# Kernel tuning notes

Hardware: AMD Instinct MI355X
Metric: run time of the kernel (lower is better)

The kernel has to match this reference:

```python
import jax, jax.numpy as jnp
import numpy as np

HEAD = 16

def setup_inputs() -> dict:
    key = jax.random.key(0)
    kq, kk, kv = jax.random.split(key, 3)
    B, S, D = 2, 2048, 1024
    q = jax.random.normal(kq, (B, S, D), dtype=jnp.float32)
    k = jax.random.normal(kk, (B, S, D), dtype=jnp.float32)
    v = jax.random.normal(kv, (B, S, D), dtype=jnp.float32)
    return {"q": q, "k": k, "v": v}

def reference(q, k, v):
    # NOTE: the source module overwrites the projected q1/k1/v1 with the raw
    # inputs (q1 = q, etc.), so w_q/w_k/w_v/w_o never affect the output.
    B, S, D = q.shape
    H = HEAD
    hd = D // H
    # [B, S, D] -> [B, H, S, hd]
    qh = q.reshape(B, S, H, hd).transpose(0, 2, 1, 3)
    kh = k.reshape(B, S, H, hd).transpose(0, 2, 1, 3)
    vh = v.reshape(B, S, H, hd).transpose(0, 2, 1, 3)
    scale = 1.0 / jnp.sqrt(jnp.float32(hd))
    scores = jnp.einsum('bhqd,bhkd->bhqk', qh, kh) * scale  # [B, H, S, S]
    attn = jax.nn.softmax(scores, axis=-1)
    x = jnp.einsum('bhqk,bhkd->bhqd', attn, vh)             # [B, H, S, hd]
    return x.transpose(0, 2, 1, 3).reshape(B, S, D)
```

## Files before the change

### kernel.cpp

```cpp
#include <hip/hip_runtime.h>
#include <hip/hip_bf16.h>

typedef __attribute__((ext_vector_type(8)))  __bf16 bf16x8;
typedef __attribute__((ext_vector_type(4)))  __bf16 bf16x4;
typedef __attribute__((ext_vector_type(4)))  float  f32x4;
typedef __attribute__((ext_vector_type(16))) float  f32x16;

#define S_LEN    2048
#define D_MODEL  1024
#define NH       16
#define HD       64
#define QB       128
#define NTILE    32
#define NOUTER   16
#define C_SCALE  0.18033688011112042f

static __device__ __forceinline__ f32x16 mfma32(bf16x8 a, bf16x8 b, f32x16 c) {
    return __builtin_amdgcn_mfma_f32_32x32x16_bf16(a, b, c, 0, 0, 0);
}

static __device__ __forceinline__ void gload16(const void* g, void* l) {
    __builtin_amdgcn_global_load_lds(
        (const __attribute__((address_space(1))) void*)g,
        (__attribute__((address_space(3)))       void*)l, 16, 0, 0);
}

__global__ __launch_bounds__(256, 4)
void prep_kernel(const float* __restrict__ Kp, const float* __restrict__ Vp,
                 char* __restrict__ Kb, char* __restrict__ Vb)
{
    const int bid  = blockIdx.x;
    const int bh   = bid >> 5;
    const int tile = bid & 31;
    const int b = bh >> 4, h = bh & 15;
    const int tid = threadIdx.x;
    const size_t gbase = (size_t)b * S_LEN * D_MODEL + (size_t)h * HD;
    char* kout = Kb + (size_t)bid * 8192;
    char* vout = Vb + (size_t)bid * 8192;

    {
        const int krow = tid >> 2, c2 = tid & 3;
        const float* kp = Kp + gbase + (size_t)(tile * 64 + krow) * D_MODEL + c2 * 16;
        f32x4 x0 = *(const f32x4*)(kp);
        f32x4 x1 = *(const f32x4*)(kp + 4);
        f32x4 x2 = *(const f32x4*)(kp + 8);
        f32x4 x3 = *(const f32x4*)(kp + 12);
        bf16x8 f0, f1;
        #pragma unroll
        for (int j = 0; j < 4; ++j) {
            f0[j] = (__bf16)x0[j]; f0[j + 4] = (__bf16)x1[j];
            f1[j] = (__bf16)x2[j]; f1[j + 4] = (__bf16)x3[j];
        }
        const int sw = (krow & 7) << 4;
        *(bf16x8*)(kout + krow * 128 + ((c2 * 32)      ^ sw)) = f0;
        *(bf16x8*)(kout + krow * 128 + ((c2 * 32 + 16) ^ sw)) = f1;
    }
    {
        const int vkg = tid >> 4, vdg = tid & 15;
        const float* vp = Vp + gbase + (size_t)(tile * 64 + vkg * 4) * D_MODEL + vdg * 4;
        f32x4 r0 = *(const f32x4*)(vp);
        f32x4 r1 = *(const f32x4*)(vp + D_MODEL);
        f32x4 r2 = *(const f32x4*)(vp + 2 * D_MODEL);
        f32x4 r3 = *(const f32x4*)(vp + 3 * D_MODEL);
        const int kvoff = 8 * ((vkg >> 1) & 1) + 16 * (vkg & 1) + 32 * (vkg >> 2);
        #pragma unroll
        for (int c = 0; c < 4; ++c) {
            const int d = vdg * 4 + c;
            bf16x4 pk;
            pk[0] = (__bf16)r0[c]; pk[1] = (__bf16)r1[c];
            pk[2] = (__bf16)r2[c]; pk[3] = (__bf16)r3[c];
            *(bf16x4*)(vout + d * 128 + (kvoff ^ ((d & 7) << 4))) = pk;
        }
    }
}

__global__ __launch_bounds__(1024, 4)
void attn_kernel(const float* __restrict__ Qp, const char* __restrict__ Kb,
                 const char* __restrict__ Vb, float* __restrict__ Op)
{
    __shared__ __align__(16) char smem[65536];

    const int bid = blockIdx.x;
    const int bh = bid & 31, qtile = bid >> 5;
    const int b = bh >> 4, h = bh & 15;
    const int tid = threadIdx.x;
    const int w = tid >> 6, lane = tid & 63;
    const int ql = lane & 31, hi = lane >> 5;
    const int qs = w & 3, kq = w >> 2;

    const size_t gbase = (size_t)b * S_LEN * D_MODEL + (size_t)h * HD;

    bf16x8 qf[4];
    {
        const int qrow = qtile * QB + qs * 32 + ql;
        const float* qp = Qp + gbase + (size_t)qrow * D_MODEL + hi * 8;
        #pragma unroll
        for (int ks = 0; ks < 4; ++ks) {
            f32x4 a = *(const f32x4*)(qp + ks * 16);
            f32x4 c = *(const f32x4*)(qp + ks * 16 + 4);
            bf16x8 f;
            #pragma unroll
            for (int j = 0; j < 4; ++j) {
                f[j]     = (__bf16)(a[j] * C_SCALE);
                f[j + 4] = (__bf16)(c[j] * C_SCALE);
            }
            qf[ks] = f;
        }
    }

    const char* kg0 = Kb + (size_t)(bh * NTILE) * 8192;
    const char* vg0 = Vb + (size_t)(bh * NTILE) * 8192;

    auto stage = [&](int db, int t) {
        const char* kg = kg0 + (size_t)t * 16384;
        const char* vg = vg0 + (size_t)t * 16384;
        char* kl = smem + db * 16384;
        char* vl = smem + 32768 + db * 16384;
        const int o = w * 1024;
        gload16(kg + o + lane * 16, kl + o);
        gload16(vg + o + lane * 16, vl + o);
    };

    const int tb = (kq >> 1) * 8192;
    const int rl = 32 * (kq & 1);
    const int vc = 64 * (kq & 1);

    f32x16 oa = {0,0,0,0,0,0,0,0,0,0,0,0,0,0,0,0};
    f32x16 ob = {0,0,0,0,0,0,0,0,0,0,0,0,0,0,0,0};
    f32x4 l4 = {0.f, 0.f, 0.f, 0.f};

    stage(0, 0);
    int cur = 0;
    for (int t = 0; t < NOUTER; ++t) {
        __syncthreads();
        if (t + 1 < NOUTER) stage(cur ^ 1, t + 1);

        const char* kl = smem + cur * 16384 + tb;
        const char* vl = smem + 32768 + cur * 16384 + tb;

        f32x16 s = {0,0,0,0,0,0,0,0,0,0,0,0,0,0,0,0};
        __builtin_amdgcn_s_setprio(1);
        #pragma unroll
        for (int ks = 0; ks < 4; ++ks) {
            const int row = rl + ql;
            bf16x8 k0 = *(const bf16x8*)(kl + row * 128 +
                            ((32 * ks + 16 * hi) ^ ((ql & 7) << 4)));
            s = mfma32(k0, qf[ks], s);
        }
        __builtin_amdgcn_s_setprio(0);

        bf16x8 pa[2];
        {
            float p[16];
            #pragma unroll
            for (int i = 0; i < 16; ++i) {
                p[i] = __builtin_amdgcn_exp2f(s[i]);
                l4[i & 3] += p[i];
            }
            #pragma unroll
            for (int z = 0; z < 2; ++z) {
                bf16x8 f;
                #pragma unroll
                for (int j = 0; j < 8; ++j) f[j] = (__bf16)p[z * 8 + j];
                pa[z] = f;
            }
        }

        __builtin_amdgcn_s_setprio(1);
        #pragma unroll
        for (int ks2 = 0; ks2 < 2; ++ks2) {
            const int col = vc + 32 * ks2 + 16 * hi;
            const int d0 = ql, d1 = 32 + ql;
            bf16x8 v0 = *(const bf16x8*)(vl + d0 * 128 + (col ^ ((d0 & 7) << 4)));
            bf16x8 v1 = *(const bf16x8*)(vl + d1 * 128 + (col ^ ((d1 & 7) << 4)));
            oa = mfma32(pa[ks2], v0, oa);
            ob = mfma32(pa[ks2], v1, ob);
        }
        __builtin_amdgcn_s_setprio(0);
        cur ^= 1;
    }

    float lsum = (l4[0] + l4[1]) + (l4[2] + l4[3]);
    lsum += __shfl_xor(lsum, 32);
    __syncthreads();
    float* lbuf  = (float*)smem;
    float* lbuf2 = (float*)(smem + 2048);
    float* obuf  = (float*)(smem + 4096);
    if (lane < 32) lbuf[kq * 128 + qs * 32 + ql] = lsum;
    __syncthreads();
    if (kq == 1) {
        if (lane < 32) {
            const int idx = qs * 32 + ql;
            lbuf2[idx] = lbuf[idx] + lbuf[128 + idx] + lbuf[256 + idx] + lbuf[384 + idx];
        }
        #pragma unroll
        for (int i = 0; i < 16; ++i) {
            const int qloc = (i & 3) + 8 * (i >> 2) + 4 * hi;
            obuf[qs * 2048 + qloc * 64 + ql]      = oa[i];
            obuf[qs * 2048 + qloc * 64 + 32 + ql] = ob[i];
        }
    }
    __syncthreads();
    if (kq == 0) {
        #pragma unroll
        for (int i = 0; i < 16; ++i) {
            const int qloc = (i & 3) + 8 * (i >> 2) + 4 * hi;
            oa[i] += obuf[qs * 2048 + qloc * 64 + ql];
            ob[i] += obuf[qs * 2048 + qloc * 64 + 32 + ql];
        }
    }
    __syncthreads();
    if (kq == 2) {
        #pragma unroll
        for (int i = 0; i < 16; ++i) {
            const int qloc = (i & 3) + 8 * (i >> 2) + 4 * hi;
            obuf[qs * 2048 + qloc * 64 + ql]      = oa[i];
            obuf[qs * 2048 + qloc * 64 + 32 + ql] = ob[i];
        }
    }
    __syncthreads();
    if (kq == 0) {
        #pragma unroll
        for (int i = 0; i < 16; ++i) {
            const int qloc = (i & 3) + 8 * (i >> 2) + 4 * hi;
            oa[i] += obuf[qs * 2048 + qloc * 64 + ql];
            ob[i] += obuf[qs * 2048 + qloc * 64 + 32 + ql];
        }
    }
    __syncthreads();
    if (kq == 3) {
        #pragma unroll
        for (int i = 0; i < 16; ++i) {
            const int qloc = (i & 3) + 8 * (i >> 2) + 4 * hi;
            obuf[qs * 2048 + qloc * 64 + ql]      = oa[i];
            obuf[qs * 2048 + qloc * 64 + 32 + ql] = ob[i];
        }
    }
    __syncthreads();
    if (kq == 0) {
        #pragma unroll
        for (int i = 0; i < 16; ++i) {
            const int qloc = (i & 3) + 8 * (i >> 2) + 4 * hi;
            const float inv = 1.0f / lbuf2[qs * 32 + qloc];
            const float v0 = (oa[i] + obuf[qs * 2048 + qloc * 64 + ql])      * inv;
            const float v1 = (ob[i] + obuf[qs * 2048 + qloc * 64 + 32 + ql]) * inv;
            float* op = Op + gbase + (size_t)(qtile * QB + qs * 32 + qloc) * D_MODEL;
            op[ql]      = v0;
            op[32 + ql] = v1;
        }
    }
}

extern "C" void kernel_launch(void* const* d_in, const int* in_sizes, int n_in,
                              void* d_out, int out_size, void* d_ws, size_t ws_size,
                              hipStream_t stream) {
    const float* q = (const float*)d_in[0];
    const float* k = (const float*)d_in[1];
    const float* v = (const float*)d_in[2];
    float* out = (float*)d_out;
    char* Kb = (char*)d_ws;
    char* Vb = (char*)d_ws + 8 * 1024 * 1024;

    prep_kernel<<<dim3(32 * NTILE), dim3(256), 0, stream>>>(k, v, Kb, Vb);
    attn_kernel<<<dim3(32 * (S_LEN / QB)), dim3(1024), 0, stream>>>(q, Kb, Vb, out);
}
```

Measured before the change: 64.00 us.

## Halve block to 512 threads with each wave computing two query sub-tiles

Each wave now handles 64 query rows (two 32-row sub-tiles) instead of 32, so every K and V fragment read from LDS feeds two MFMAs. The block shrinks to 8 waves, each staging twice as many bytes per tile. The change targets LDS read traffic per MFMA and the cost of the cross-wave reduction. In exchange, register pressure roughly doubles for accumulators and Q fragments, and resident waves per CU drop. The normalisation sum is now computed inline at the final write instead of in a separate buffer.

New measurement: 63.25 us. No clear change (-1.2%).

```diff
diff --git a/kernel.cpp b/kernel.cpp
--- a/kernel.cpp
+++ b/kernel.cpp
@@ -74,7 +74,7 @@
     }
 }
 
-__global__ __launch_bounds__(1024, 4)
+__global__ __launch_bounds__(512, 3)
 void attn_kernel(const float* __restrict__ Qp, const char* __restrict__ Kb,
                  const char* __restrict__ Vb, float* __restrict__ Op)
 {
@@ -86,25 +86,26 @@
     const int tid = threadIdx.x;
     const int w = tid >> 6, lane = tid & 63;
     const int ql = lane & 31, hi = lane >> 5;
-    const int qs = w & 3, kq = w >> 2;
+    const int qp = w & 1, kq = w >> 1;
 
     const size_t gbase = (size_t)b * S_LEN * D_MODEL + (size_t)h * HD;
 
-    bf16x8 qf[4];
-    {
-        const int qrow = qtile * QB + qs * 32 + ql;
-        const float* qp = Qp + gbase + (size_t)qrow * D_MODEL + hi * 8;
+    bf16x8 qf[2][4];
+    #pragma unroll
+    for (int sub = 0; sub < 2; ++sub) {
+        const int qrow = qtile * QB + qp * 64 + sub * 32 + ql;
+        const float* qp_ = Qp + gbase + (size_t)qrow * D_MODEL + hi * 8;
         #pragma unroll
         for (int ks = 0; ks < 4; ++ks) {
-            f32x4 a = *(const f32x4*)(qp + ks * 16);
-            f32x4 c = *(const f32x4*)(qp + ks * 16 + 4);
+            f32x4 a = *(const f32x4*)(qp_ + ks * 16);
+            f32x4 c = *(const f32x4*)(qp_ + ks * 16 + 4);
             bf16x8 f;
             #pragma unroll
             for (int j = 0; j < 4; ++j) {
                 f[j]     = (__bf16)(a[j] * C_SCALE);
                 f[j + 4] = (__bf16)(c[j] * C_SCALE);
             }
-            qf[ks] = f;
+            qf[sub][ks] = f;
         }
     }
 
@@ -116,18 +117,39 @@
         const char* vg = vg0 + (size_t)t * 16384;
         char* kl = smem + db * 16384;
         char* vl = smem + 32768 + db * 16384;
-        const int o = w * 1024;
-        gload16(kg + o + lane * 16, kl + o);
-        gload16(vg + o + lane * 16, vl + o);
+        const int o0 = w * 2048, o1 = w * 2048 + 1024;
+        gload16(kg + o0 + lane * 16, kl + o0);
+        gload16(kg + o1 + lane * 16, kl + o1);
+        gload16(vg + o0 + lane * 16, vl + o0);
+        gload16(vg + o1 + lane * 16, vl + o1);
     };
 
     const int tb = (kq >> 1) * 8192;
     const int rl = 32 * (kq & 1);
     const int vc = 64 * (kq & 1);
 
-    f32x16 oa = {0,0,0,0,0,0,0,0,0,0,0,0,0,0,0,0};
-    f32x16 ob = {0,0,0,0,0,0,0,0,0,0,0,0,0,0,0,0};
-    f32x4 l4 = {0.f, 0.f, 0.f, 0.f};
+    f32x16 oa0 = {0,0,0,0,0,0,0,0,0,0,0,0,0,0,0,0};
+    f32x16 ob0 = {0,0,0,0,0,0,0,0,0,0,0,0,0,0,0,0};
+    f32x16 oa1 = {0,0,0,0,0,0,0,0,0,0,0,0,0,0,0,0};
+    f32x16 ob1 = {0,0,0,0,0,0,0,0,0,0,0,0,0,0,0,0};
+    f32x4 l4a = {0.f, 0.f, 0.f, 0.f};
+    f32x4 l4b = {0.f, 0.f, 0.f, 0.f};
+
+    auto soft = [](const f32x16& sv, bf16x8* dst, f32x4& lacc) {
+        float p[16];
+        #pragma unroll
+        for (int i = 0; i < 16; ++i) {
+            p[i] = __builtin_amdgcn_exp2f(sv[i]);
+            lacc[i & 3] += p[i];
+        }
+        #pragma unroll
+        for (int z = 0; z < 2; ++z) {
+            bf16x8 f;
+            #pragma unroll
+            for (int j = 0; j < 8; ++j) f[j] = (__bf16)p[z * 8 + j];
+            dst[z] = f;
+        }
+    };
 
     stage(0, 0);
     int cur = 0;
@@ -138,33 +160,22 @@
         const char* kl = smem + cur * 16384 + tb;
         const char* vl = smem + 32768 + cur * 16384 + tb;
 
-        f32x16 s = {0,0,0,0,0,0,0,0,0,0,0,0,0,0,0,0};
+        f32x16 s0 = {0,0,0,0,0,0,0,0,0,0,0,0,0,0,0,0};
+        f32x16 s1 = {0,0,0,0,0,0,0,0,0,0,0,0,0,0,0,0};
         __builtin_amdgcn_s_setprio(1);
         #pragma unroll
         for (int ks = 0; ks < 4; ++ks) {
             const int row = rl + ql;
             bf16x8 k0 = *(const bf16x8*)(kl + row * 128 +
-                            ((32 * ks + 16 * hi) ^ ((ql & 7) << 4)));
-            s = mfma32(k0, qf[ks], s);
+                            ((32 * ks + 16 * hi) ^ ((row & 7) << 4)));
+            s0 = mfma32(k0, qf[0][ks], s0);
+            s1 = mfma32(k0, qf[1][ks], s1);
         }
         __builtin_amdgcn_s_setprio(0);
 
-        bf16x8 pa[2];
-        {
-            float p[16];
-            #pragma unroll
-            for (int i = 0; i < 16; ++i) {
-                p[i] = __builtin_amdgcn_exp2f(s[i]);
-                l4[i & 3] += p[i];
-            }
-            #pragma unroll
-            for (int z = 0; z < 2; ++z) {
-                bf16x8 f;
-                #pragma unroll
-                for (int j = 0; j < 8; ++j) f[j] = (__bf16)p[z * 8 + j];
-                pa[z] = f;
-            }
-        }
+        bf16x8 pa0[2], pa1[2];
+        soft(s0, pa0, l4a);
+        soft(s1, pa1, l4b);
 
         __builtin_amdgcn_s_setprio(1);
         #pragma unroll
@@ -173,31 +184,36 @@
             const int d0 = ql, d1 = 32 + ql;
             bf16x8 v0 = *(const bf16x8*)(vl + d0 * 128 + (col ^ ((d0 & 7) << 4)));
             bf16x8 v1 = *(const bf16x8*)(vl + d1 * 128 + (col ^ ((d1 & 7) << 4)));
-            oa = mfma32(pa[ks2], v0, oa);
-            ob = mfma32(pa[ks2], v1, ob);
+            oa0 = mfma32(pa0[ks2], v0, oa0);
+            ob0 = mfma32(pa0[ks2], v1, ob0);
+            oa1 = mfma32(pa1[ks2], v0, oa1);
+            ob1 = mfma32(pa1[ks2], v1, ob1);
         }
         __builtin_amdgcn_s_setprio(0);
         cur ^= 1;
     }
 
-    float lsum = (l4[0] + l4[1]) + (l4[2] + l4[3]);
-    lsum += __shfl_xor(lsum, 32);
-    __syncthreads();
-    float* lbuf  = (float*)smem;
-    float* lbuf2 = (float*)(smem + 2048);
-    float* obuf  = (float*)(smem + 4096);
-    if (lane < 32) lbuf[kq * 128 + qs * 32 + ql] = lsum;
+    float lsA = (l4a[0] + l4a[1]) + (l4a[2] + l4a[3]);
+    float lsB = (l4b[0] + l4b[1]) + (l4b[2] + l4b[3]);
+    lsA += __shfl_xor(lsA, 32);
+    lsB += __shfl_xor(lsB, 32);
+    __syncthreads();
+    float* obuf = (float*)smem;
+    float* lbuf = (float*)(smem + 32768);
+    if (lane < 32) {
+        lbuf[kq * 128 + qp * 64 + ql]      = lsA;
+        lbuf[kq * 128 + qp * 64 + 32 + ql] = lsB;
+    }
     __syncthreads();
     if (kq == 1) {
-        if (lane < 32) {
-            const int idx = qs * 32 + ql;
-            lbuf2[idx] = lbuf[idx] + lbuf[128 + idx] + lbuf[256 + idx] + lbuf[384 + idx];
-        }
-        #pragma unroll
-        for (int i = 0; i < 16; ++i) {
-            const int qloc = (i & 3) + 8 * (i >> 2) + 4 * hi;
-            obuf[qs * 2048 + qloc * 64 + ql]      = oa[i];
-            obuf[qs * 2048 + qloc * 64 + 32 + ql] = ob[i];
+        #pragma unroll
+        for (int i = 0; i < 16; ++i) {
+            const int qloc = (i & 3) + 8 * (i >> 2) + 4 * hi;
+            float* ob_ = obuf + qp * 4096;
+            ob_[qloc * 64 + ql]             = oa0[i];
+            ob_[qloc * 64 + 32 + ql]        = ob0[i];
+            ob_[(32 + qloc) * 64 + ql]      = oa1[i];
+            ob_[(32 + qloc) * 64 + 32 + ql] = ob1[i];
         }
     }
     __syncthreads();
@@ -205,8 +221,11 @@
         #pragma unroll
         for (int i = 0; i < 16; ++i) {
             const int qloc = (i & 3) + 8 * (i >> 2) + 4 * hi;
-            oa[i] += obuf[qs * 2048 + qloc * 64 + ql];
-            ob[i] += obuf[qs * 2048 + qloc * 64 + 32 + ql];
+            const float* ob_ = obuf + qp * 4096;
+            oa0[i] += ob_[qloc * 64 + ql];
+            ob0[i] += ob_[qloc * 64 + 32 + ql];
+            oa1[i] += ob_[(32 + qloc) * 64 + ql];
+            ob1[i] += ob_[(32 + qloc) * 64 + 32 + ql];
         }
     }
     __syncthreads();
@@ -214,8 +233,11 @@
         #pragma unroll
         for (int i = 0; i < 16; ++i) {
             const int qloc = (i & 3) + 8 * (i >> 2) + 4 * hi;
-            obuf[qs * 2048 + qloc * 64 + ql]      = oa[i];
-            obuf[qs * 2048 + qloc * 64 + 32 + ql] = ob[i];
+            float* ob_ = obuf + qp * 4096;
+            ob_[qloc * 64 + ql]             = oa0[i];
+            ob_[qloc * 64 + 32 + ql]        = ob0[i];
+            ob_[(32 + qloc) * 64 + ql]      = oa1[i];
+            ob_[(32 + qloc) * 64 + 32 + ql] = ob1[i];
         }
     }
     __syncthreads();
@@ -223,8 +245,11 @@
         #pragma unroll
         for (int i = 0; i < 16; ++i) {
             const int qloc = (i & 3) + 8 * (i >> 2) + 4 * hi;
-            oa[i] += obuf[qs * 2048 + qloc * 64 + ql];
-            ob[i] += obuf[qs * 2048 + qloc * 64 + 32 + ql];
+            const float* ob_ = obuf + qp * 4096;
+            oa0[i] += ob_[qloc * 64 + ql];
+            ob0[i] += ob_[qloc * 64 + 32 + ql];
+            oa1[i] += ob_[(32 + qloc) * 64 + ql];
+            ob1[i] += ob_[(32 + qloc) * 64 + 32 + ql];
         }
     }
     __syncthreads();
@@ -232,8 +257,11 @@
         #pragma unroll
         for (int i = 0; i < 16; ++i) {
             const int qloc = (i & 3) + 8 * (i >> 2) + 4 * hi;
-            obuf[qs * 2048 + qloc * 64 + ql]      = oa[i];
-            obuf[qs * 2048 + qloc * 64 + 32 + ql] = ob[i];
+            float* ob_ = obuf + qp * 4096;
+            ob_[qloc * 64 + ql]             = oa0[i];
+            ob_[qloc * 64 + 32 + ql]        = ob0[i];
+            ob_[(32 + qloc) * 64 + ql]      = oa1[i];
+            ob_[(32 + qloc) * 64 + 32 + ql] = ob1[i];
         }
     }
     __syncthreads();
@@ -241,12 +269,18 @@
         #pragma unroll
         for (int i = 0; i < 16; ++i) {
             const int qloc = (i & 3) + 8 * (i >> 2) + 4 * hi;
-            const float inv = 1.0f / lbuf2[qs * 32 + qloc];
-            const float v0 = (oa[i] + obuf[qs * 2048 + qloc * 64 + ql])      * inv;
-            const float v1 = (ob[i] + obuf[qs * 2048 + qloc * 64 + 32 + ql]) * inv;
-            float* op = Op + gbase + (size_t)(qtile * QB + qs * 32 + qloc) * D_MODEL;
-            op[ql]      = v0;
-            op[32 + ql] = v1;
+            const float* ob_ = obuf + qp * 4096;
+            const int qa = qp * 64 + qloc;
+            const float ltA = lbuf[qa] + lbuf[128 + qa] + lbuf[256 + qa] + lbuf[384 + qa];
+            const float ltB = lbuf[32 + qa] + lbuf[160 + qa] + lbuf[288 + qa] + lbuf[416 + qa];
+            const float invA = 1.0f / ltA;
+            const float invB = 1.0f / ltB;
+            float* opA = Op + gbase + (size_t)(qtile * QB + qa) * D_MODEL;
+            float* opB = Op + gbase + (size_t)(qtile * QB + qa + 32) * D_MODEL;
+            opA[ql]      = (oa0[i] + ob_[qloc * 64 + ql])             * invA;
+            opA[32 + ql] = (ob0[i] + ob_[qloc * 64 + 32 + ql])        * invA;
+            opB[ql]      = (oa1[i] + ob_[(32 + qloc) * 64 + ql])      * invB;
+            opB[32 + ql] = (ob1[i] + ob_[(32 + qloc) * 64 + 32 + ql]) * invB;
         }
     }
 }
@@ -262,5 +296,5 @@
     char* Vb = (char*)d_ws + 8 * 1024 * 1024;
 
     prep_kernel<<<dim3(32 * NTILE), dim3(256), 0, stream>>>(k, v, Kb, Vb);
-    attn_kernel<<<dim3(32 * (S_LEN / QB)), dim3(1024), 0, stream>>>(q, Kb, Vb, out);
-}
+    attn_kernel<<<dim3(32 * (S_LEN / QB)), dim3(512), 0, stream>>>(q, Kb, Vb, out);
+}
```

## Read K/V tiles directly from global memory with smaller query blocks

Applied to the files above, without the earlier changes.

Drops the LDS double-buffered staging of K/V tiles through global_load_lds. Each wave now reads its pre-swizzled bf16 K/V fragments straight from global memory, relying on the L2/L1 caches. Query blocks shrink from 128 to 32 rows with 256-thread workgroups, so there are four times as many blocks and no per-tile barriers. The cost is that each block re-reads K/V from cache for every 32 query rows, which adds cache traffic and exposes global-load latency that the LDS pipeline used to hide.

Result: slower. 91.99 us (+43.7%).

```diff
diff --git a/kernel.cpp b/kernel.cpp
--- a/kernel.cpp
+++ b/kernel.cpp
@@ -10,19 +10,12 @@
 #define D_MODEL  1024
 #define NH       16
 #define HD       64
-#define QB       128
+#define QB       32
 #define NTILE    32
-#define NOUTER   16
 #define C_SCALE  0.18033688011112042f
 
 static __device__ __forceinline__ f32x16 mfma32(bf16x8 a, bf16x8 b, f32x16 c) {
     return __builtin_amdgcn_mfma_f32_32x32x16_bf16(a, b, c, 0, 0, 0);
-}
-
-static __device__ __forceinline__ void gload16(const void* g, void* l) {
-    __builtin_amdgcn_global_load_lds(
-        (const __attribute__((address_space(1))) void*)g,
-        (__attribute__((address_space(3)))       void*)l, 16, 0, 0);
 }
 
 __global__ __launch_bounds__(256, 4)
@@ -74,11 +67,12 @@
     }
 }
 
-__global__ __launch_bounds__(1024, 4)
+__global__ __launch_bounds__(256, 4)
 void attn_kernel(const float* __restrict__ Qp, const char* __restrict__ Kb,
                  const char* __restrict__ Vb, float* __restrict__ Op)
 {
-    __shared__ __align__(16) char smem[65536];
+    __shared__ float lbuf[4 * 32];
+    __shared__ __align__(16) float obuf[32 * 64];
 
     const int bid = blockIdx.x;
     const int bh = bid & 31, qtile = bid >> 5;
@@ -86,18 +80,18 @@
     const int tid = threadIdx.x;
     const int w = tid >> 6, lane = tid & 63;
     const int ql = lane & 31, hi = lane >> 5;
-    const int qs = w & 3, kq = w >> 2;
+    const int kq = w;
 
     const size_t gbase = (size_t)b * S_LEN * D_MODEL + (size_t)h * HD;
 
     bf16x8 qf[4];
     {
-        const int qrow = qtile * QB + qs * 32 + ql;
-        const float* qp = Qp + gbase + (size_t)qrow * D_MODEL + hi * 8;
+        const int qrow = qtile * QB + ql;
+        const float* qp_ = Qp + gbase + (size_t)qrow * D_MODEL + hi * 8;
         #pragma unroll
         for (int ks = 0; ks < 4; ++ks) {
-            f32x4 a = *(const f32x4*)(qp + ks * 16);
-            f32x4 c = *(const f32x4*)(qp + ks * 16 + 4);
+            f32x4 a = *(const f32x4*)(qp_ + ks * 16);
+            f32x4 c = *(const f32x4*)(qp_ + ks * 16 + 4);
             bf16x8 f;
             #pragma unroll
             for (int j = 0; j < 4; ++j) {
@@ -108,43 +102,27 @@
         }
     }
 
-    const char* kg0 = Kb + (size_t)(bh * NTILE) * 8192;
-    const char* vg0 = Vb + (size_t)(bh * NTILE) * 8192;
-
-    auto stage = [&](int db, int t) {
-        const char* kg = kg0 + (size_t)t * 16384;
-        const char* vg = vg0 + (size_t)t * 16384;
-        char* kl = smem + db * 16384;
-        char* vl = smem + 32768 + db * 16384;
-        const int o = w * 1024;
-        gload16(kg + o + lane * 16, kl + o);
-        gload16(vg + o + lane * 16, vl + o);
-    };
-
-    const int tb = (kq >> 1) * 8192;
-    const int rl = 32 * (kq & 1);
-    const int vc = 64 * (kq & 1);
+    const char* kg = Kb + (size_t)(bh * NTILE + kq * 8) * 8192;
+    const char* vg = Vb + (size_t)(bh * NTILE + kq * 8) * 8192;
 
     f32x16 oa = {0,0,0,0,0,0,0,0,0,0,0,0,0,0,0,0};
     f32x16 ob = {0,0,0,0,0,0,0,0,0,0,0,0,0,0,0,0};
     f32x4 l4 = {0.f, 0.f, 0.f, 0.f};
 
-    stage(0, 0);
-    int cur = 0;
-    for (int t = 0; t < NOUTER; ++t) {
-        __syncthreads();
-        if (t + 1 < NOUTER) stage(cur ^ 1, t + 1);
-
-        const char* kl = smem + cur * 16384 + tb;
-        const char* vl = smem + 32768 + cur * 16384 + tb;
+    #pragma unroll 2
+    for (int t = 0; t < 16; ++t) {
+        const char* kt = kg + (t >> 1) * 8192;
+        const char* vt = vg + (t >> 1) * 8192;
+        const int half = t & 1;
+        const int row  = 32 * half + ql;
+        const int vc   = 64 * half;
 
         f32x16 s = {0,0,0,0,0,0,0,0,0,0,0,0,0,0,0,0};
         __builtin_amdgcn_s_setprio(1);
         #pragma unroll
         for (int ks = 0; ks < 4; ++ks) {
-            const int row = rl + ql;
-            bf16x8 k0 = *(const bf16x8*)(kl + row * 128 +
-                            ((32 * ks + 16 * hi) ^ ((ql & 7) << 4)));
+            bf16x8 k0 = *(const bf16x8*)(kt + row * 128 +
+                            ((32 * ks + 16 * hi) ^ ((row & 7) << 4)));
             s = mfma32(k0, qf[ks], s);
         }
         __builtin_amdgcn_s_setprio(0);
@@ -170,34 +148,24 @@
         #pragma unroll
         for (int ks2 = 0; ks2 < 2; ++ks2) {
             const int col = vc + 32 * ks2 + 16 * hi;
-            const int d0 = ql, d1 = 32 + ql;
-            bf16x8 v0 = *(const bf16x8*)(vl + d0 * 128 + (col ^ ((d0 & 7) << 4)));
-            bf16x8 v1 = *(const bf16x8*)(vl + d1 * 128 + (col ^ ((d1 & 7) << 4)));
+            bf16x8 v0 = *(const bf16x8*)(vt + ql * 128 + (col ^ ((ql & 7) << 4)));
+            bf16x8 v1 = *(const bf16x8*)(vt + (32 + ql) * 128 + (col ^ ((ql & 7) << 4)));
             oa = mfma32(pa[ks2], v0, oa);
             ob = mfma32(pa[ks2], v1, ob);
         }
         __builtin_amdgcn_s_setprio(0);
-        cur ^= 1;
     }
 
     float lsum = (l4[0] + l4[1]) + (l4[2] + l4[3]);
     lsum += __shfl_xor(lsum, 32);
-    __syncthreads();
-    float* lbuf  = (float*)smem;
-    float* lbuf2 = (float*)(smem + 2048);
-    float* obuf  = (float*)(smem + 4096);
-    if (lane < 32) lbuf[kq * 128 + qs * 32 + ql] = lsum;
+    if (lane < 32) lbuf[kq * 32 + ql] = lsum;
     __syncthreads();
     if (kq == 1) {
-        if (lane < 32) {
-            const int idx = qs * 32 + ql;
-            lbuf2[idx] = lbuf[idx] + lbuf[128 + idx] + lbuf[256 + idx] + lbuf[384 + idx];
-        }
-        #pragma unroll
-        for (int i = 0; i < 16; ++i) {
-            const int qloc = (i & 3) + 8 * (i >> 2) + 4 * hi;
-            obuf[qs * 2048 + qloc * 64 + ql]      = oa[i];
-            obuf[qs * 2048 + qloc * 64 + 32 + ql] = ob[i];
+        #pragma unroll
+        for (int i = 0; i < 16; ++i) {
+            const int qloc = (i & 3) + 8 * (i >> 2) + 4 * hi;
+            obuf[qloc * 64 + ql]      = oa[i];
+            obuf[qloc * 64 + 32 + ql] = ob[i];
         }
     }
     __syncthreads();
@@ -205,8 +173,8 @@
         #pragma unroll
         for (int i = 0; i < 16; ++i) {
             const int qloc = (i & 3) + 8 * (i >> 2) + 4 * hi;
-            oa[i] += obuf[qs * 2048 + qloc * 64 + ql];
-            ob[i] += obuf[qs * 2048 + qloc * 64 + 32 + ql];
+            oa[i] += obuf[qloc * 64 + ql];
+            ob[i] += obuf[qloc * 64 + 32 + ql];
         }
     }
     __syncthreads();
@@ -214,8 +182,8 @@
         #pragma unroll
         for (int i = 0; i < 16; ++i) {
             const int qloc = (i & 3) + 8 * (i >> 2) + 4 * hi;
-            obuf[qs * 2048 + qloc * 64 + ql]      = oa[i];
-            obuf[qs * 2048 + qloc * 64 + 32 + ql] = ob[i];
+            obuf[qloc * 64 + ql]      = oa[i];
+            obuf[qloc * 64 + 32 + ql] = ob[i];
         }
     }
     __syncthreads();
@@ -223,8 +191,8 @@
         #pragma unroll
         for (int i = 0; i < 16; ++i) {
             const int qloc = (i & 3) + 8 * (i >> 2) + 4 * hi;
-            oa[i] += obuf[qs * 2048 + qloc * 64 + ql];
-            ob[i] += obuf[qs * 2048 + qloc * 64 + 32 + ql];
+            oa[i] += obuf[qloc * 64 + ql];
+            ob[i] += obuf[qloc * 64 + 32 + ql];
         }
     }
     __syncthreads();
@@ -232,8 +200,8 @@
         #pragma unroll
         for (int i = 0; i < 16; ++i) {
             const int qloc = (i & 3) + 8 * (i >> 2) + 4 * hi;
-            obuf[qs * 2048 + qloc * 64 + ql]      = oa[i];
-            obuf[qs * 2048 + qloc * 64 + 32 + ql] = ob[i];
+            obuf[qloc * 64 + ql]      = oa[i];
+            obuf[qloc * 64 + 32 + ql] = ob[i];
         }
     }
     __syncthreads();
@@ -241,12 +209,12 @@
         #pragma unroll
         for (int i = 0; i < 16; ++i) {
             const int qloc = (i & 3) + 8 * (i >> 2) + 4 * hi;
-            const float inv = 1.0f / lbuf2[qs * 32 + qloc];
-            const float v0 = (oa[i] + obuf[qs * 2048 + qloc * 64 + ql])      * inv;
-            const float v1 = (ob[i] + obuf[qs * 2048 + qloc * 64 + 32 + ql]) * inv;
-            float* op = Op + gbase + (size_t)(qtile * QB + qs * 32 + qloc) * D_MODEL;
-            op[ql]      = v0;
-            op[32 + ql] = v1;
+            const float lt = lbuf[qloc] + lbuf[32 + qloc] +
+                             lbuf[64 + qloc] + lbuf[96 + qloc];
+            const float inv = 1.0f / lt;
+            float* op = Op + gbase + (size_t)(qtile * QB + qloc) * D_MODEL;
+            op[ql]      = (oa[i] + obuf[qloc * 64 + ql])      * inv;
+            op[32 + ql] = (ob[i] + obuf[qloc * 64 + 32 + ql]) * inv;
         }
     }
 }
@@ -262,5 +230,5 @@
     char* Vb = (char*)d_ws + 8 * 1024 * 1024;
 
     prep_kernel<<<dim3(32 * NTILE), dim3(256), 0, stream>>>(k, v, Kb, Vb);
-    attn_kernel<<<dim3(32 * (S_LEN / QB)), dim3(1024), 0, stream>>>(q, Kb, Vb, out);
-}
+    attn_kernel<<<dim3(32 * (S_LEN / QB)), dim3(256), 0, stream>>>(q, Kb, Vb, out);
+}
```
